# Performance work log

Hardware: AMD Instinct MI355X
Metric: run time of the kernel (lower is better)

Reference implementation:

```python
import jax, jax.numpy as jnp
import numpy as np

N_NODES = 50000
N_EDGES = 640000
IN, HID, OUT = 128, 128, 40


def _sage_conv(x, src, dst, W_l, b_l, W_r, num_nodes):
    """PyG SAGEConv (aggr='mean', root_weight=True):
       out_i = mean_{j in N(i)} x_j @ W_l^T + b_l + x_i @ W_r^T
    """
    msgs = x[src]  # [E, d] gather over source nodes
    agg = jax.ops.segment_sum(msgs, dst, num_segments=num_nodes)  # [N, d]
    deg = jax.ops.segment_sum(jnp.ones((src.shape[0],), x.dtype), dst,
                              num_segments=num_nodes)  # [N]
    mean = agg / jnp.maximum(deg, 1.0)[:, None]
    return mean @ W_l.T + b_l + x @ W_r.T


def setup_inputs() -> dict:
    key = jax.random.key(0)
    ks = jax.random.split(key, 12)
    x = jax.random.normal(ks[0], (N_NODES, IN), dtype=jnp.float32)
    edge_index = jax.random.randint(ks[1], (2, N_EDGES), 0, N_NODES, dtype=jnp.int64)

    def lin(k, fan_out, fan_in):
        s = 1.0 / np.sqrt(fan_in)
        return jax.random.uniform(k, (fan_out, fan_in), jnp.float32, -s, s)

    return {
        "x": x,
        "edge_index": edge_index,
        "W1l": lin(ks[2], HID, IN),  "b1": jnp.zeros((HID,), jnp.float32), "W1r": lin(ks[3], HID, IN),
        "W2l": lin(ks[4], HID, HID), "b2": jnp.zeros((HID,), jnp.float32), "W2r": lin(ks[5], HID, HID),
        "W3l": lin(ks[6], OUT, HID), "b3": jnp.zeros((OUT,), jnp.float32), "W3r": lin(ks[7], OUT, HID),
    }


def reference(x, edge_index, W1l, b1, W1r, W2l, b2, W2r, W3l, b3, W3r):
    src, dst = edge_index[0], edge_index[1]
    n = x.shape[0]
    # Dropout is identity in eval mode; reference is the deterministic forward.
    h = _sage_conv(x, src, dst, W1l, b1, W1r, n)
    h = jax.nn.relu(h)
    h = _sage_conv(h, src, dst, W2l, b2, W2r, n)
    h = jax.nn.relu(h)
    h = _sage_conv(h, src, dst, W3l, b3, W3r, n)
    return jax.nn.log_softmax(h, axis=-1)
```

## Files before the change

kernel.cpp:

```cpp
#include <hip/hip_runtime.h>

#define NN 50000
#define NE 640000
#define NBUCK 196
#define NSB 157
#define EPB 4096
#define EPT 16
#define BCAP 4096
#define FDIM 128
#define FOUT 40

typedef unsigned int uint;
typedef unsigned short ushort;
typedef unsigned char uchar;
typedef __attribute__((ext_vector_type(8))) __bf16 bf16x8;
typedef __attribute__((ext_vector_type(4))) float f32x4;
typedef __attribute__((ext_vector_type(2))) float f32x2;

union BF8 { bf16x8 v; uint4 u; ushort s[8]; };

__device__ __forceinline__ ushort f2bf(float f){
  uint b = __float_as_uint(f);
  b += 0x7fffu + ((b >> 16) & 1u);
  return (ushort)(b >> 16);
}
__device__ __forceinline__ float bflo(uint v){ return __uint_as_float(v << 16); }
__device__ __forceinline__ float bfhi(uint v){ return __uint_as_float(v & 0xffff0000u); }
__device__ __forceinline__ uint pack2(float a, float b){
  return (uint)f2bf(a) | ((uint)f2bf(b) << 16);
}
__device__ __forceinline__ int get_edge(const void* ep, int is64, int idx){
  return is64 ? (int)(((const long long*)ep)[idx]) : ((const int*)ep)[idx];
}

__device__ __forceinline__ uint fp8enc(float f){
  uint b = __float_as_uint(f);
  uint s = (b >> 24) & 0x80u;
  float af = __uint_as_float(b & 0x7fffffffu);
  if(af < 0.015625f){
    uint m = (uint)__float2int_rn(af * 512.0f);
    return (m == 8u) ? (s | 0x08u) : (s | m);
  }
  uint ab = __float_as_uint(af);
  ab += 0x7ffffu + ((ab >> 20) & 1u);
  int e = (int)(ab >> 23) - 120;
  uint m = (ab >> 20) & 7u;
  if(e > 15){ e = 15; m = 6u; }
  return s | ((uint)e << 3) | m;
}
__device__ __forceinline__ float fp8dec(uint byte){
  uint s = (byte & 0x80u) << 24;
  uint e = (byte >> 3) & 15u;
  uint m = byte & 7u;
  float nrm = __uint_as_float(s | ((e + 120u) << 23) | (m << 20));
  float den = __uint_as_float(s | __float_as_uint((float)m * 0.001953125f));
  return e ? nrm : den;
}
__device__ __forceinline__ void fp8add4(uint dw, float* a){
#if __has_builtin(__builtin_amdgcn_cvt_pk_f32_fp8)
  f32x2 p0 = __builtin_amdgcn_cvt_pk_f32_fp8((int)dw, false);
  f32x2 p1 = __builtin_amdgcn_cvt_pk_f32_fp8((int)dw, true);
  a[0] += p0[0]; a[1] += p0[1]; a[2] += p1[0]; a[3] += p1[1];
#else
  a[0] += fp8dec(dw & 0xffu);
  a[1] += fp8dec((dw >> 8) & 0xffu);
  a[2] += fp8dec((dw >> 16) & 0xffu);
  a[3] += fp8dec(dw >> 24);
#endif
}

__launch_bounds__(256)
__global__ void k_pre(const float* __restrict__ x,
                      const float* __restrict__ W1l, const float* __restrict__ W1r,
                      const float* __restrict__ b1,
                      uchar* __restrict__ u8, ushort* __restrict__ v,
                      const unsigned long long* __restrict__ e64,
                      int* __restrict__ flag, int* __restrict__ gcur){
  if(blockIdx.x >= 625){
    int t = threadIdx.x;
    if(t < NBUCK) gcur[t] = 0;
    if(t < 64){
      unsigned long long vv = e64[t];
      int ok = (int)__all(vv < 4294967296ULL);
      if(t == 0) *flag = ok;
    }
    return;
  }
  int g = threadIdx.x >> 6;
  int l = threadIdx.x & 63;
  int worker = blockIdx.x;
  int r16 = l & 15, q = l >> 4;

  BF8 bl[2][4], br[2][4];
#pragma unroll
  for(int tt = 0; tt < 2; ++tt){
    int colw = 32 * g + 16 * tt + r16;
    const float* pl = W1l + colw * FDIM + q * 8;
    const float* pr = W1r + colw * FDIM + q * 8;
#pragma unroll
    for(int ks = 0; ks < 4; ++ks){
      float4 x0 = *(const float4*)(pl + 32 * ks);
      float4 x1 = *(const float4*)(pl + 32 * ks + 4);
      BF8 t;
      t.s[0]=f2bf(x0.x); t.s[1]=f2bf(x0.y); t.s[2]=f2bf(x0.z); t.s[3]=f2bf(x0.w);
      t.s[4]=f2bf(x1.x); t.s[5]=f2bf(x1.y); t.s[6]=f2bf(x1.z); t.s[7]=f2bf(x1.w);
      bl[tt][ks] = t;
      float4 y0 = *(const float4*)(pr + 32 * ks);
      float4 y1 = *(const float4*)(pr + 32 * ks + 4);
      BF8 w;
      w.s[0]=f2bf(y0.x); w.s[1]=f2bf(y0.y); w.s[2]=f2bf(y0.z); w.s[3]=f2bf(y0.w);
      w.s[4]=f2bf(y1.x); w.s[5]=f2bf(y1.y); w.s[6]=f2bf(y1.z); w.s[7]=f2bf(y1.w);
      br[tt][ks] = w;
    }
  }
  float bv0 = b1[32 * g + r16];
  float bv1 = b1[32 * g + 16 + r16];

  for(int s = 0; s < 5; ++s){
    int m0 = (worker * 5 + s) * 16;
    BF8 a[4];
    const float* pf = x + (size_t)(m0 + r16) * FDIM + q * 8;
#pragma unroll
    for(int ks = 0; ks < 4; ++ks){
      float4 x0 = *(const float4*)(pf + 32 * ks);
      float4 x1 = *(const float4*)(pf + 32 * ks + 4);
      BF8 t;
      t.s[0]=f2bf(x0.x); t.s[1]=f2bf(x0.y); t.s[2]=f2bf(x0.z); t.s[3]=f2bf(x0.w);
      t.s[4]=f2bf(x1.x); t.s[5]=f2bf(x1.y); t.s[6]=f2bf(x1.z); t.s[7]=f2bf(x1.w);
      a[ks] = t;
    }
    f32x4 aU0 = {0,0,0,0}, aU1 = {0,0,0,0}, aV0 = {0,0,0,0}, aV1 = {0,0,0,0};
#pragma unroll
    for(int ks = 0; ks < 4; ++ks){
      aU0 = __builtin_amdgcn_mfma_f32_16x16x32_bf16(a[ks].v, bl[0][ks].v, aU0, 0, 0, 0);
      aV0 = __builtin_amdgcn_mfma_f32_16x16x32_bf16(a[ks].v, br[0][ks].v, aV0, 0, 0, 0);
      aU1 = __builtin_amdgcn_mfma_f32_16x16x32_bf16(a[ks].v, bl[1][ks].v, aU1, 0, 0, 0);
      aV1 = __builtin_amdgcn_mfma_f32_16x16x32_bf16(a[ks].v, br[1][ks].v, aV1, 0, 0, 0);
    }
#pragma unroll
    for(int r = 0; r < 4; ++r){
      size_t row = (size_t)(m0 + q * 4 + r);
      u8[row * FDIM + 32 * g + r16]      = (uchar)fp8enc(aU0[r]);
      u8[row * FDIM + 32 * g + 16 + r16] = (uchar)fp8enc(aU1[r]);
      v[row * FDIM + 32 * g + r16]       = f2bf(aV0[r] + bv0);
      v[row * FDIM + 32 * g + 16 + r16]  = f2bf(aV1[r] + bv1);
    }
  }
}

__launch_bounds__(256)
__global__ void k_scatter(const void* __restrict__ edges, const int* __restrict__ flag,
                          int* __restrict__ gcur, uint* __restrict__ recbuf){
  __shared__ int cnt[NBUCK], off[NBUCK], cur[NBUCK], gb[NBUCK];
  __shared__ int s[256];
  __shared__ int nTot_s;
  __shared__ uint recLds[EPB];
  int t = threadIdx.x, sb = blockIdx.x;
  for(int i = t; i < NBUCK; i += 256) cnt[i] = 0;
  __syncthreads();
  int is64 = *flag;
  uint recs[EPT];
  int e0 = sb * EPB + t;
#pragma unroll
  for(int i = 0; i < EPT; ++i){
    int e = e0 + i * 256;
    if(e < NE){
      uint sn = (uint)get_edge(edges, is64, e);
      uint d  = (uint)get_edge(edges, is64, NE + e);
      recs[i] = (d << 16) | sn;
      atomicAdd(&cnt[d >> 8], 1);
    } else recs[i] = 0xFFFFFFFFu;
  }
  __syncthreads();
  int v = (t < NBUCK) ? cnt[t] : 0;
  s[t] = v; __syncthreads();
  for(int o = 1; o < 256; o <<= 1){
    int a = (t >= o) ? s[t - o] : 0;
    __syncthreads(); s[t] += a; __syncthreads();
  }
  if(t < NBUCK){
    off[t] = s[t] - v; cur[t] = 0;
    gb[t] = v ? atomicAdd(&gcur[t], v) : 0;
  }
  if(t == 255) nTot_s = s[255];
  __syncthreads();
#pragma unroll
  for(int i = 0; i < EPT; ++i){
    uint r = recs[i];
    if(r != 0xFFFFFFFFu){
      int b = (int)(r >> 24);
      int q = off[b] + atomicAdd(&cur[b], 1);
      recLds[q] = r;
    }
  }
  __syncthreads();
  int nTot = nTot_s;
  for(int q = t; q < nTot; q += 256){
    uint r = recLds[q];
    int b = (int)(r >> 24);
    recbuf[(size_t)b * BCAP + gb[b] + (q - off[b])] = r;
  }
}

__global__ void k_csr(const uint* __restrict__ recbuf, const int* __restrict__ gcur,
                      int* __restrict__ rp, int* __restrict__ degN,
                      int* __restrict__ col){
  __shared__ int cnt[256], rpl[256], cur[256];
  __shared__ int s[256];
  __shared__ int colL[BCAP];
  int t = threadIdx.x, b = blockIdx.x;
  int base = b * BCAP, n = gcur[b];
  cnt[t] = 0; __syncthreads();
  for(int q = t; q < n; q += 256) atomicAdd(&cnt[(recbuf[base + q] >> 16) & 255], 1);
  __syncthreads();
  int v = cnt[t];
  s[t] = v; __syncthreads();
  for(int o = 1; o < 256; o <<= 1){
    int a = (t >= o) ? s[t - o] : 0;
    __syncthreads(); s[t] += a; __syncthreads();
  }
  rpl[t] = s[t] - v; cur[t] = 0;
  int node = b * 256 + t;
  if(node < NN){ rp[node] = base + rpl[t]; degN[node] = v; }
  __syncthreads();
  for(int q = t; q < n; q += 256){
    uint r = recbuf[base + q];
    int dl = (r >> 16) & 255;
    int p = rpl[dl] + atomicAdd(&cur[dl], 1);
    colL[p] = (int)(r & 0xFFFFu);
  }
  __syncthreads();
  for(int q = t; q < n; q += 256) col[base + q] = colL[q];
}

__global__ void k_aggv8(const uchar* __restrict__ u8, const ushort* __restrict__ v,
                        const int* __restrict__ rp, const int* __restrict__ degN,
                        const int* __restrict__ col, ushort* __restrict__ h){
  int node = (blockIdx.x * blockDim.x + threadIdx.x) >> 6;
  if(node >= NN) return;
  int l = threadIdx.x & 63;
  int c8 = l & 7, eg = l >> 3;
  int beg = rp[node], deg = degN[node];
  float acc[16];
#pragma unroll
  for(int i = 0; i < 16; ++i) acc[i] = 0.f;
  const uchar* fbase = u8 + c8 * 16;

  for(int base = 0; base < deg; base += 64){
    int nchunk = min(deg - base, 64);
    int idx = col[beg + base + min(l, nchunk - 1)];
#pragma unroll 2
    for(int j = 0; j < nchunk; j += 8){
      int e = j + eg;
      int s = __shfl(idx, min(e, nchunk - 1));
      uint4 w = *(const uint4*)(fbase + (size_t)s * FDIM);
      if(e < nchunk){
        fp8add4(w.x, acc + 0);
        fp8add4(w.y, acc + 4);
        fp8add4(w.z, acc + 8);
        fp8add4(w.w, acc + 12);
      }
    }
  }
#pragma unroll
  for(int i = 0; i < 16; ++i){
    acc[i] += __shfl_xor(acc[i], 8);
    acc[i] += __shfl_xor(acc[i], 16);
    acc[i] += __shfl_xor(acc[i], 32);
  }
  if(eg == 0){
    float inv = 1.0f / (float)max(deg, 1);
    const ushort* pv = v + (size_t)node * FDIM + c8 * 16;
    uint4 v0 = *(const uint4*)(pv);
    uint4 v1 = *(const uint4*)(pv + 8);
    uint4 o0, o1;
    o0.x = pack2(fmaxf(acc[0]*inv  + bflo(v0.x), 0.f), fmaxf(acc[1]*inv  + bfhi(v0.x), 0.f));
    o0.y = pack2(fmaxf(acc[2]*inv  + bflo(v0.y), 0.f), fmaxf(acc[3]*inv  + bfhi(v0.y), 0.f));
    o0.z = pack2(fmaxf(acc[4]*inv  + bflo(v0.z), 0.f), fmaxf(acc[5]*inv  + bfhi(v0.z), 0.f));
    o0.w = pack2(fmaxf(acc[6]*inv  + bflo(v0.w), 0.f), fmaxf(acc[7]*inv  + bfhi(v0.w), 0.f));
    o1.x = pack2(fmaxf(acc[8]*inv  + bflo(v1.x), 0.f), fmaxf(acc[9]*inv  + bfhi(v1.x), 0.f));
    o1.y = pack2(fmaxf(acc[10]*inv + bflo(v1.y), 0.f), fmaxf(acc[11]*inv + bfhi(v1.y), 0.f));
    o1.z = pack2(fmaxf(acc[12]*inv + bflo(v1.z), 0.f), fmaxf(acc[13]*inv + bfhi(v1.z), 0.f));
    o1.w = pack2(fmaxf(acc[14]*inv + bflo(v1.w), 0.f), fmaxf(acc[15]*inv + bfhi(v1.w), 0.f));
    ushort* ph = h + (size_t)node * FDIM + c8 * 16;
    *(uint4*)(ph)     = o0;
    *(uint4*)(ph + 8) = o1;
  }
}

__launch_bounds__(256)
__global__ void k_linuv2(const ushort* __restrict__ inB,
                         const float* __restrict__ Wl, const float* __restrict__ Wr,
                         const float* __restrict__ bias,
                         uchar* __restrict__ u8, ushort* __restrict__ v){
  int g = threadIdx.x >> 6;
  int l = threadIdx.x & 63;
  int worker = blockIdx.x;
  int r16 = l & 15, q = l >> 4;

  BF8 bl[2][4], br[2][4];
#pragma unroll
  for(int tt = 0; tt < 2; ++tt){
    int colw = 32 * g + 16 * tt + r16;
    const float* pl = Wl + colw * FDIM + q * 8;
    const float* pr = Wr + colw * FDIM + q * 8;
#pragma unroll
    for(int ks = 0; ks < 4; ++ks){
      float4 x0 = *(const float4*)(pl + 32 * ks);
      float4 x1 = *(const float4*)(pl + 32 * ks + 4);
      BF8 t;
      t.s[0]=f2bf(x0.x); t.s[1]=f2bf(x0.y); t.s[2]=f2bf(x0.z); t.s[3]=f2bf(x0.w);
      t.s[4]=f2bf(x1.x); t.s[5]=f2bf(x1.y); t.s[6]=f2bf(x1.z); t.s[7]=f2bf(x1.w);
      bl[tt][ks] = t;
      float4 y0 = *(const float4*)(pr + 32 * ks);
      float4 y1 = *(const float4*)(pr + 32 * ks + 4);
      BF8 w;
      w.s[0]=f2bf(y0.x); w.s[1]=f2bf(y0.y); w.s[2]=f2bf(y0.z); w.s[3]=f2bf(y0.w);
      w.s[4]=f2bf(y1.x); w.s[5]=f2bf(y1.y); w.s[6]=f2bf(y1.z); w.s[7]=f2bf(y1.w);
      br[tt][ks] = w;
    }
  }
  float bv0 = bias[32 * g + r16];
  float bv1 = bias[32 * g + 16 + r16];

  for(int s = 0; s < 5; ++s){
    int m0 = (worker * 5 + s) * 16;
    BF8 a[4];
    const ushort* pb = inB + (size_t)(m0 + r16) * FDIM + q * 8;
#pragma unroll
    for(int ks = 0; ks < 4; ++ks) a[ks].u = *(const uint4*)(pb + 32 * ks);
    f32x4 aU0 = {0,0,0,0}, aU1 = {0,0,0,0}, aV0 = {0,0,0,0}, aV1 = {0,0,0,0};
#pragma unroll
    for(int ks = 0; ks < 4; ++ks){
      aU0 = __builtin_amdgcn_mfma_f32_16x16x32_bf16(a[ks].v, bl[0][ks].v, aU0, 0, 0, 0);
      aV0 = __builtin_amdgcn_mfma_f32_16x16x32_bf16(a[ks].v, br[0][ks].v, aV0, 0, 0, 0);
      aU1 = __builtin_amdgcn_mfma_f32_16x16x32_bf16(a[ks].v, bl[1][ks].v, aU1, 0, 0, 0);
      aV1 = __builtin_amdgcn_mfma_f32_16x16x32_bf16(a[ks].v, br[1][ks].v, aV1, 0, 0, 0);
    }
#pragma unroll
    for(int r = 0; r < 4; ++r){
      size_t row = (size_t)(m0 + q * 4 + r);
      u8[row * FDIM + 32 * g + r16]      = (uchar)fp8enc(aU0[r]);
      u8[row * FDIM + 32 * g + 16 + r16] = (uchar)fp8enc(aU1[r]);
      v[row * FDIM + 32 * g + r16]       = f2bf(aV0[r] + bv0);
      v[row * FDIM + 32 * g + 16 + r16]  = f2bf(aV1[r] + bv1);
    }
  }
}

__launch_bounds__(192)
__global__ void k_linuv40(const ushort* __restrict__ inB,
                          const float* __restrict__ Wl, const float* __restrict__ Wr,
                          const float* __restrict__ bias,
                          ushort* __restrict__ u3, ushort* __restrict__ v3){
  int g = threadIdx.x >> 6;
  int l = threadIdx.x & 63;
  int worker = blockIdx.x;
  int r16 = l & 15, q = l >> 4;
  int colw = 16 * g + r16;
  bool vcol = colw < FOUT;

  BF8 bl[4], br[4];
#pragma unroll
  for(int ks = 0; ks < 4; ++ks){
    BF8 t, w;
    if(vcol){
      const float* pl = Wl + colw * FDIM + q * 8 + 32 * ks;
      const float* pr = Wr + colw * FDIM + q * 8 + 32 * ks;
      float4 x0 = ((const float4*)pl)[0], x1 = ((const float4*)pl)[1];
      t.s[0]=f2bf(x0.x); t.s[1]=f2bf(x0.y); t.s[2]=f2bf(x0.z); t.s[3]=f2bf(x0.w);
      t.s[4]=f2bf(x1.x); t.s[5]=f2bf(x1.y); t.s[6]=f2bf(x1.z); t.s[7]=f2bf(x1.w);
      float4 y0 = ((const float4*)pr)[0], y1 = ((const float4*)pr)[1];
      w.s[0]=f2bf(y0.x); w.s[1]=f2bf(y0.y); w.s[2]=f2bf(y0.z); w.s[3]=f2bf(y0.w);
      w.s[4]=f2bf(y1.x); w.s[5]=f2bf(y1.y); w.s[6]=f2bf(y1.z); w.s[7]=f2bf(y1.w);
    } else {
      t.u = make_uint4(0,0,0,0);
      w.u = make_uint4(0,0,0,0);
    }
    bl[ks] = t; br[ks] = w;
  }
  float bv = vcol ? bias[colw] : 0.f;

  for(int s = 0; s < 5; ++s){
    int m0 = (worker * 5 + s) * 16;
    BF8 a[4];
    const ushort* pb = inB + (size_t)(m0 + r16) * FDIM + q * 8;
#pragma unroll
    for(int ks = 0; ks < 4; ++ks) a[ks].u = *(const uint4*)(pb + 32 * ks);
    f32x4 aU = {0,0,0,0}, aV = {0,0,0,0};
#pragma unroll
    for(int ks = 0; ks < 4; ++ks){
      aU = __builtin_amdgcn_mfma_f32_16x16x32_bf16(a[ks].v, bl[ks].v, aU, 0, 0, 0);
      aV = __builtin_amdgcn_mfma_f32_16x16x32_bf16(a[ks].v, br[ks].v, aV, 0, 0, 0);
    }
    if(vcol){
#pragma unroll
      for(int r = 0; r < 4; ++r){
        size_t row = (size_t)(m0 + q * 4 + r);
        u3[row * FOUT + colw] = f2bf(aU[r]);
        v3[row * FOUT + colw] = f2bf(aV[r] + bv);
      }
    }
  }
}

__global__ void k_agg40(const ushort* __restrict__ u3, const ushort* __restrict__ v3,
                        const int* __restrict__ rp, const int* __restrict__ degN,
                        const int* __restrict__ col, float* __restrict__ out){
  int node = (blockIdx.x * blockDim.x + threadIdx.x) >> 6;
  if(node >= NN) return;
  int l = threadIdx.x & 63;
  int c = l % 20, sl = l / 20;
  const ushort* fbase = u3 + 2 * c;

  int beg = rp[node], deg = degN[node];
  float a0 = 0.f, a1 = 0.f;
  for(int base = 0; base < deg; base += 60){
    int nchunk = min(deg - base, 60);
    int idx = col[beg + base + min(l, nchunk - 1)];
#pragma unroll 2
    for(int j = 0; j < nchunk; j += 3){
      int e = j + sl;
      int s = __shfl(idx, min(e, nchunk - 1));
      uint w = *(const uint*)(fbase + (size_t)s * FOUT);
      if(sl < 3 && e < nchunk){
        a0 += bflo(w); a1 += bfhi(w);
      }
    }
  }
  a0 += __shfl(a0, l + 20) + __shfl(a0, l + 40);
  a1 += __shfl(a1, l + 20) + __shfl(a1, l + 40);

  float inv = 1.0f / (float)max(deg, 1);
  float z0 = 0.f, z1 = 0.f;
  if(l < 20){
    uint vv = *(const uint*)(v3 + (size_t)node * FOUT + 2 * c);
    z0 = a0 * inv + bflo(vv);
    z1 = a1 * inv + bfhi(vv);
  }
  float m = (l < 20) ? fmaxf(z0, z1) : -1e30f;
#pragma unroll
  for(int d = 1; d < 64; d <<= 1) m = fmaxf(m, __shfl_xor(m, d));
  float es = (l < 20) ? (__expf(z0 - m) + __expf(z1 - m)) : 0.f;
#pragma unroll
  for(int d = 1; d < 64; d <<= 1) es += __shfl_xor(es, d);
  float lse = m + __logf(es);
  if(l < 20){
    *(float2*)(out + (size_t)node * FOUT + 2 * c) = make_float2(z0 - lse, z1 - lse);
  }
}

extern "C" void kernel_launch(void* const* d_in, const int* in_sizes, int n_in,
                              void* d_out, int out_size, void* d_ws, size_t ws_size,
                              hipStream_t stream){
  const float* x   = (const float*)d_in[0];
  const void*  edges = d_in[1];
  const float* W1l = (const float*)d_in[2];
  const float* b1  = (const float*)d_in[3];
  const float* W1r = (const float*)d_in[4];
  const float* W2l = (const float*)d_in[5];
  const float* b2  = (const float*)d_in[6];
  const float* W2r = (const float*)d_in[7];
  const float* W3l = (const float*)d_in[8];
  const float* b3  = (const float*)d_in[9];
  const float* W3r = (const float*)d_in[10];
  float* out = (float*)d_out;

  char* ws = (char*)d_ws;
  size_t off = 0;
  auto alloc = [&](size_t bytes)->void*{
    void* p = ws + off;
    off += (bytes + 255) & ~(size_t)255;
    return p;
  };
  ushort* u    = (ushort*)alloc((size_t)NN * FDIM * 2);
  ushort* v    = (ushort*)alloc((size_t)NN * FDIM * 2);
  ushort* h    = (ushort*)alloc((size_t)NN * FDIM * 2);
  ushort* h2   = (ushort*)alloc((size_t)NN * FDIM * 2);
  int*    rp   = (int*)alloc((size_t)NN * 4);
  int*    degN = (int*)alloc((size_t)NN * 4);
  int*    col  = (int*)alloc((size_t)NBUCK * BCAP * 4);
  uint*   recbuf = (uint*)alloc((size_t)NBUCK * BCAP * 4);
  int*    gcur = (int*)alloc((size_t)NBUCK * 4);
  int*    flag = (int*)alloc(256);
  uchar*  u8   = (uchar*)u;

  int aggGrid = (NN * 64 + 255) / 256;
  k_pre<<<626, 256, 0, stream>>>(x, W1l, W1r, b1, u8, v,
                                 (const unsigned long long*)edges, flag, gcur);
  k_scatter<<<NSB, 256, 0, stream>>>(edges, flag, gcur, recbuf);
  k_csr<<<NBUCK, 256, 0, stream>>>(recbuf, gcur, rp, degN, col);

  k_aggv8<<<aggGrid, 256, 0, stream>>>(u8, v, rp, degN, col, h);
  k_linuv2<<<625, 256, 0, stream>>>(h, W2l, W2r, b2, u8, v);
  k_aggv8<<<aggGrid, 256, 0, stream>>>(u8, v, rp, degN, col, h2);
  k_linuv40<<<625, 192, 0, stream>>>(h2, W3l, W3r, b3, u, v);
  k_agg40<<<aggGrid, 256, 0, stream>>>(u, v, rp, degN, col, out);
}
```

Baseline: 185.8 us.

## Fuse edge bucketing scatter into first-layer projection kernel and unroll gathers

Merges the edge scatter/bucketing kernel into the layer-1 projection kernel as extra blocks, so the bucketing runs concurrently with the dense MFMA work instead of as a separate launch. The 64-bit edge detection moves into each scatter block, and bucket counters are zeroed with a memset. The gather loops in the aggregation kernels are unrolled 4 instead of 2 to keep more loads in flight. The fused kernel now reserves the scatter blocks' large LDS allocation for every block, which may lower occupancy of the projection blocks.

Result: faster. 181.2 us (-2.5%).

```diff
diff --git a/kernel.cpp b/kernel.cpp
--- a/kernel.cpp
+++ b/kernel.cpp
@@ -70,19 +70,66 @@
 }
 
 __launch_bounds__(256)
-__global__ void k_pre(const float* __restrict__ x,
-                      const float* __restrict__ W1l, const float* __restrict__ W1r,
-                      const float* __restrict__ b1,
-                      uchar* __restrict__ u8, ushort* __restrict__ v,
-                      const unsigned long long* __restrict__ e64,
-                      int* __restrict__ flag, int* __restrict__ gcur){
+__global__ void k_front(const float* __restrict__ x,
+                        const float* __restrict__ W1l, const float* __restrict__ W1r,
+                        const float* __restrict__ b1,
+                        uchar* __restrict__ u8, ushort* __restrict__ v,
+                        const void* __restrict__ edges,
+                        int* __restrict__ gcur, uint* __restrict__ recbuf){
   if(blockIdx.x >= 625){
-    int t = threadIdx.x;
-    if(t < NBUCK) gcur[t] = 0;
+    __shared__ int cnt[NBUCK], off[NBUCK], cur[NBUCK], gb[NBUCK];
+    __shared__ int s[256];
+    __shared__ int nTot_s, is64_s;
+    __shared__ uint recLds[EPB];
+    int t = threadIdx.x, sb = blockIdx.x - 625;
+    for(int i = t; i < NBUCK; i += 256) cnt[i] = 0;
     if(t < 64){
-      unsigned long long vv = e64[t];
+      unsigned long long vv = ((const unsigned long long*)edges)[t];
       int ok = (int)__all(vv < 4294967296ULL);
-      if(t == 0) *flag = ok;
+      if(t == 0) is64_s = ok;
+    }
+    __syncthreads();
+    int is64 = is64_s;
+    uint recs[EPT];
+    int e0 = sb * EPB + t;
+#pragma unroll
+    for(int i = 0; i < EPT; ++i){
+      int e = e0 + i * 256;
+      if(e < NE){
+        uint sn = (uint)get_edge(edges, is64, e);
+        uint d  = (uint)get_edge(edges, is64, NE + e);
+        recs[i] = (d << 16) | sn;
+        atomicAdd(&cnt[d >> 8], 1);
+      } else recs[i] = 0xFFFFFFFFu;
+    }
+    __syncthreads();
+    int vv = (t < NBUCK) ? cnt[t] : 0;
+    s[t] = vv; __syncthreads();
+    for(int o = 1; o < 256; o <<= 1){
+      int a = (t >= o) ? s[t - o] : 0;
+      __syncthreads(); s[t] += a; __syncthreads();
+    }
+    if(t < NBUCK){
+      off[t] = s[t] - vv; cur[t] = 0;
+      gb[t] = vv ? atomicAdd(&gcur[t], vv) : 0;
+    }
+    if(t == 255) nTot_s = s[255];
+    __syncthreads();
+#pragma unroll
+    for(int i = 0; i < EPT; ++i){
+      uint r = recs[i];
+      if(r != 0xFFFFFFFFu){
+        int b = (int)(r >> 24);
+        int q = off[b] + atomicAdd(&cur[b], 1);
+        recLds[q] = r;
+      }
+    }
+    __syncthreads();
+    int nTot = nTot_s;
+    for(int q = t; q < nTot; q += 256){
+      uint r = recLds[q];
+      int b = (int)(r >> 24);
+      recbuf[(size_t)b * BCAP + gb[b] + (q - off[b])] = r;
     }
     return;
   }
@@ -145,60 +192,6 @@
       v[row * FDIM + 32 * g + r16]       = f2bf(aV0[r] + bv0);
       v[row * FDIM + 32 * g + 16 + r16]  = f2bf(aV1[r] + bv1);
     }
-  }
-}
-
-__launch_bounds__(256)
-__global__ void k_scatter(const void* __restrict__ edges, const int* __restrict__ flag,
-                          int* __restrict__ gcur, uint* __restrict__ recbuf){
-  __shared__ int cnt[NBUCK], off[NBUCK], cur[NBUCK], gb[NBUCK];
-  __shared__ int s[256];
-  __shared__ int nTot_s;
-  __shared__ uint recLds[EPB];
-  int t = threadIdx.x, sb = blockIdx.x;
-  for(int i = t; i < NBUCK; i += 256) cnt[i] = 0;
-  __syncthreads();
-  int is64 = *flag;
-  uint recs[EPT];
-  int e0 = sb * EPB + t;
-#pragma unroll
-  for(int i = 0; i < EPT; ++i){
-    int e = e0 + i * 256;
-    if(e < NE){
-      uint sn = (uint)get_edge(edges, is64, e);
-      uint d  = (uint)get_edge(edges, is64, NE + e);
-      recs[i] = (d << 16) | sn;
-      atomicAdd(&cnt[d >> 8], 1);
-    } else recs[i] = 0xFFFFFFFFu;
-  }
-  __syncthreads();
-  int v = (t < NBUCK) ? cnt[t] : 0;
-  s[t] = v; __syncthreads();
-  for(int o = 1; o < 256; o <<= 1){
-    int a = (t >= o) ? s[t - o] : 0;
-    __syncthreads(); s[t] += a; __syncthreads();
-  }
-  if(t < NBUCK){
-    off[t] = s[t] - v; cur[t] = 0;
-    gb[t] = v ? atomicAdd(&gcur[t], v) : 0;
-  }
-  if(t == 255) nTot_s = s[255];
-  __syncthreads();
-#pragma unroll
-  for(int i = 0; i < EPT; ++i){
-    uint r = recs[i];
-    if(r != 0xFFFFFFFFu){
-      int b = (int)(r >> 24);
-      int q = off[b] + atomicAdd(&cur[b], 1);
-      recLds[q] = r;
-    }
-  }
-  __syncthreads();
-  int nTot = nTot_s;
-  for(int q = t; q < nTot; q += 256){
-    uint r = recLds[q];
-    int b = (int)(r >> 24);
-    recbuf[(size_t)b * BCAP + gb[b] + (q - off[b])] = r;
   }
 }
 
@@ -249,7 +242,7 @@
   for(int base = 0; base < deg; base += 64){
     int nchunk = min(deg - base, 64);
     int idx = col[beg + base + min(l, nchunk - 1)];
-#pragma unroll 2
+#pragma unroll 4
     for(int j = 0; j < nchunk; j += 8){
       int e = j + eg;
       int s = __shfl(idx, min(e, nchunk - 1));
@@ -418,7 +411,7 @@
   for(int base = 0; base < deg; base += 60){
     int nchunk = min(deg - base, 60);
     int idx = col[beg + base + min(l, nchunk - 1)];
-#pragma unroll 2
+#pragma unroll 4
     for(int j = 0; j < nchunk; j += 3){
       int e = j + sl;
       int s = __shfl(idx, min(e, nchunk - 1));
@@ -482,13 +475,11 @@
   int*    col  = (int*)alloc((size_t)NBUCK * BCAP * 4);
   uint*   recbuf = (uint*)alloc((size_t)NBUCK * BCAP * 4);
   int*    gcur = (int*)alloc((size_t)NBUCK * 4);
-  int*    flag = (int*)alloc(256);
   uchar*  u8   = (uchar*)u;
 
   int aggGrid = (NN * 64 + 255) / 256;
-  k_pre<<<626, 256, 0, stream>>>(x, W1l, W1r, b1, u8, v,
-                                 (const unsigned long long*)edges, flag, gcur);
-  k_scatter<<<NSB, 256, 0, stream>>>(edges, flag, gcur, recbuf);
+  hipMemsetAsync(gcur, 0, NBUCK * 4, stream);
+  k_front<<<625 + NSB, 256, 0, stream>>>(x, W1l, W1r, b1, u8, v, edges, gcur, recbuf);
   k_csr<<<NBUCK, 256, 0, stream>>>(recbuf, gcur, rp, degN, col);
 
   k_aggv8<<<aggGrid, 256, 0, stream>>>(u8, v, rp, degN, col, h);
```
